# Kernel tuning notes

Hardware: AMD Instinct MI355X
Metric: run time of the kernel (lower is better)

## Reference

```python
import jax, jax.numpy as jnp
import numpy as np
from jax import lax

TOP_K = 4  # n_expert_per_token


def setup_inputs() -> dict:
    key = jax.random.key(0)
    ks = jax.random.split(key, 9)
    B, S, D, F, E = 2, 512, 1024, 2048, 32
    sD = 1.0 / np.sqrt(D)
    sF = 1.0 / np.sqrt(F)
    return {
        "x": jax.random.normal(ks[0], (B, S, D), jnp.float32),
        "gate_w": jax.random.normal(ks[1], (E, D), jnp.float32) * sD,
        "expert_bias": jax.random.normal(ks[2], (E,), jnp.float32) * 0.01,
        "wg": jax.random.normal(ks[3], (E, F, D), jnp.float32) * sD,
        "wu": jax.random.normal(ks[4], (E, F, D), jnp.float32) * sD,
        "wd": jax.random.normal(ks[5], (E, D, F), jnp.float32) * sF,
        "ws_g": jax.random.normal(ks[6], (F, D), jnp.float32) * sD,
        "ws_u": jax.random.normal(ks[7], (F, D), jnp.float32) * sD,
        "ws_d": jax.random.normal(ks[8], (D, F), jnp.float32) * sF,
    }


def _swiglu(xf, w_gate, w_up, w_down):
    # xf: [T, D]; w_gate/w_up: [F, D]; w_down: [D, F]
    h = jax.nn.silu(xf @ w_gate.T) * (xf @ w_up.T)
    return h @ w_down.T


def reference(x, gate_w, expert_bias, wg, wu, wd, ws_g, ws_u, ws_d):
    B, S, D = x.shape
    E = gate_w.shape[0]
    xf = x.reshape(-1, D)                      # [T, D]
    T = xf.shape[0]

    # shared expert (always active)
    shared = _swiglu(xf, ws_g, ws_u, ws_d)     # [T, D]

    # router: logits + load-balance bias, top-k, softmax over selected logits
    logits = xf @ gate_w.T + expert_bias       # [T, E]
    top_vals, top_idx = lax.top_k(logits, TOP_K)
    weights = jax.nn.softmax(top_vals, axis=-1)  # [T, K]

    # per-token combine weight for every expert (zero if not routed)
    cw = jnp.sum(jax.nn.one_hot(top_idx, E, dtype=weights.dtype) * weights[..., None], axis=1)  # [T, E]

    # dense-masked expert compute: scan over experts, accumulate weighted outputs
    def body(acc, p):
        wg_e, wu_e, wd_e, cw_e = p             # [F,D],[F,D],[D,F],[T]
        y = _swiglu(xf, wg_e, wu_e, wd_e)      # [T, D]
        return acc + cw_e[:, None] * y, None

    routed, _ = lax.scan(body, jnp.zeros_like(xf), (wg, wu, wd, cw.T))

    out = (shared + routed).reshape(B, S, D)

    # load stats (eval path; no bias update since training=False)
    counts = jnp.zeros((E,), jnp.float32).at[top_idx.reshape(-1)].add(1.0)
    load_balance = jnp.std(counts) / (jnp.mean(counts) + 1e-6)
    return out, counts, load_balance
```

## Files before the change

### kernel.cpp

```cpp
#include <hip/hip_runtime.h>
#include <hip/hip_bf16.h>
#include <math.h>

#define T_TOK 1024
#define DDIM  1024
#define FDIM  2048
#define NEXP  32
#define KTOP  4
#define ESH   33
#define RTOT  5120

#define WS_CNT   0
#define WS_NWORK 32
#define WS_OFF   34
#define WS_WL    68
#define WS_TOPI  324
#define WS_TOPW  4420
#define WS_LTOK  8516
#define WS_LW    13636
#define WS_H     18816

typedef __attribute__((ext_vector_type(8))) short short8;
typedef __attribute__((ext_vector_type(4))) float f32x4;

__device__ inline unsigned pack_bf16x2(float a, float b) {
  unsigned ua = __float_as_uint(a), ub = __float_as_uint(b);
  ua = (ua + 0x8000u) >> 16;
  ub = (ub + 0x8000u) & 0xFFFF0000u;
  return ua | ub;
}

__global__ void k_router(const float* __restrict__ x, const float* __restrict__ gw,
                         const float* __restrict__ bias, int* __restrict__ ws) {
  int t = blockIdx.x;
  int lane = threadIdx.x;
  int e = lane & 31, half = lane >> 5;
  const float* xh = x + (size_t)t * DDIM + half * (DDIM / 2);
  const float* gr = gw + (size_t)e * DDIM + half * (DDIM / 2);
  float acc = 0.f;
  for (int d = 0; d < DDIM / 2; d += 4) {
    float4 xv = *(const float4*)(xh + d);
    float4 gv = *(const float4*)(gr + d);
    acc += xv.x * gv.x + xv.y * gv.y + xv.z * gv.z + xv.w * gv.w;
  }
  acc += __shfl_xor(acc, 32, 64);
  __shared__ float lg[NEXP];
  if (lane < NEXP) lg[lane] = acc + bias[lane];
  __syncthreads();
  if (lane == 0) {
    int idx[KTOP]; float val[KTOP]; unsigned used = 0;
    for (int s = 0; s < KTOP; ++s) {
      float best = -1e30f; int bi = 0;
      for (int j = 0; j < NEXP; ++j)
        if (!((used >> j) & 1u) && lg[j] > best) { best = lg[j]; bi = j; }
      used |= 1u << bi; idx[s] = bi; val[s] = best;
    }
    float m = val[0], ssum = 0.f, w[KTOP];
    for (int s = 0; s < KTOP; ++s) { w[s] = __expf(val[s] - m); ssum += w[s]; }
    for (int s = 0; s < KTOP; ++s) {
      ws[WS_TOPI + t * KTOP + s] = idx[s];
      ((float*)ws)[WS_TOPW + t * KTOP + s] = w[s] / ssum;
      atomicAdd(&ws[WS_CNT + idx[s]], 1);
    }
  }
}

__global__ void k_post(int* __restrict__ ws, float* __restrict__ out) {
  __shared__ int off_s[ESH + 1];
  __shared__ int cur_s[ESH];
  int tid = threadIdx.x;
  if (tid == 0) {
    int o = 0;
    for (int e = 0; e < NEXP; ++e) { off_s[e] = o; o += ws[WS_CNT + e]; }
    off_s[32] = o; off_s[33] = o + T_TOK;
    int w = 0;
    for (int e = 0; e < ESH; ++e) {
      int n = (e < NEXP) ? ws[WS_CNT + e] : T_TOK;
      int tiles = (n + 31) >> 5;
      for (int mt = 0; mt < tiles; ++mt) ws[WS_WL + w++] = (e << 6) | mt;
    }
    ws[WS_NWORK] = w;
    for (int i = 0; i <= ESH; ++i) ws[WS_OFF + i] = off_s[i];
    float mean = 0.f;
    for (int e = 0; e < NEXP; ++e) mean += (float)ws[WS_CNT + e];
    mean *= (1.f / NEXP);
    float var = 0.f;
    for (int e = 0; e < NEXP; ++e) { float d = (float)ws[WS_CNT + e] - mean; var += d * d; }
    var *= (1.f / NEXP);
    for (int e = 0; e < NEXP; ++e) out[(size_t)T_TOK * DDIM + e] = (float)ws[WS_CNT + e];
    out[(size_t)T_TOK * DDIM + NEXP] = sqrtf(var) / (mean + 1e-6f);
  }
  if (tid < ESH) cur_s[tid] = 0;
  __syncthreads();
  if (tid < T_TOK) {
    for (int s = 0; s < KTOP; ++s) {
      int e = ws[WS_TOPI + tid * KTOP + s];
      int p = atomicAdd(&cur_s[e], 1);
      ws[WS_LTOK + off_s[e] + p] = tid;
      ((float*)ws)[WS_LW + off_s[e] + p] = ((const float*)ws)[WS_TOPW + tid * KTOP + s];
    }
    ws[WS_LTOK + off_s[32] + tid] = tid;
    ((float*)ws)[WS_LW + off_s[32] + tid] = 1.f;
  }
}

__global__ __launch_bounds__(256) void k_stage1(
    const float* __restrict__ x, const float* __restrict__ wg, const float* __restrict__ wu,
    const float* __restrict__ wsg, const float* __restrict__ wsu,
    const int* __restrict__ ws, __hip_bfloat16* __restrict__ H) {
  int wid = blockIdx.x;
  if (wid >= ws[WS_NWORK]) return;
  int wl = ws[WS_WL + wid];
  int e = wl >> 6, mt = wl & 63;
  int off_e = ws[WS_OFF + e];
  int n_e = ws[WS_OFF + e + 1] - off_e;
  int m0 = off_e + mt * 32;
  int nb = blockIdx.y * 64;
  const float* wgp = (e < NEXP) ? wg + (size_t)e * FDIM * DDIM : wsg;
  const float* wup = (e < NEXP) ? wu + (size_t)e * FDIM * DDIM : wsu;

  __shared__ int tok_s[32];
  __shared__ ushort a_s[8][32][8];
  __shared__ ushort bg_s[8][64][8];
  __shared__ ushort bu_s[8][64][8];

  int tid = threadIdx.x;
  if (tid < 32) {
    int idx = mt * 32 + tid;
    tok_s[tid] = ws[WS_LTOK + off_e + (idx < n_e ? idx : 0)];
  }
  __syncthreads();

  int kgA = tid & 7, mA = tid >> 3;
  const float* aptr = x + (size_t)tok_s[mA] * DDIM + kgA * 8;
  int kgB = tid & 7, nB = tid >> 3;
  f32x4 accg0 = {0,0,0,0}, accg1 = {0,0,0,0}, accu0 = {0,0,0,0}, accu1 = {0,0,0,0};
  int wave = tid >> 6, lane = tid & 63;
  int msub = wave & 1, npair = wave >> 1;
  int lm = lane & 15, lk = lane >> 4;

  for (int k0 = 0; k0 < DDIM; k0 += 64) {
    {
      float4 f0 = *(const float4*)(aptr + k0);
      float4 f1 = *(const float4*)(aptr + k0 + 4);
      uint4 p; p.x = pack_bf16x2(f0.x, f0.y); p.y = pack_bf16x2(f0.z, f0.w);
      p.z = pack_bf16x2(f1.x, f1.y); p.w = pack_bf16x2(f1.z, f1.w);
      *(uint4*)&a_s[kgA][mA][0] = p;
    }
#pragma unroll
    for (int r = 0; r < 2; ++r) {
      int n = nB + r * 32;
      const float* gsrc = wgp + (size_t)(nb + n) * DDIM + k0 + kgB * 8;
      float4 f0 = *(const float4*)gsrc; float4 f1 = *(const float4*)(gsrc + 4);
      uint4 p; p.x = pack_bf16x2(f0.x, f0.y); p.y = pack_bf16x2(f0.z, f0.w);
      p.z = pack_bf16x2(f1.x, f1.y); p.w = pack_bf16x2(f1.z, f1.w);
      *(uint4*)&bg_s[kgB][n][0] = p;
      const float* usrc = wup + (size_t)(nb + n) * DDIM + k0 + kgB * 8;
      f0 = *(const float4*)usrc; f1 = *(const float4*)(usrc + 4);
      p.x = pack_bf16x2(f0.x, f0.y); p.y = pack_bf16x2(f0.z, f0.w);
      p.z = pack_bf16x2(f1.x, f1.y); p.w = pack_bf16x2(f1.z, f1.w);
      *(uint4*)&bu_s[kgB][n][0] = p;
    }
    __syncthreads();
#pragma unroll
    for (int ks = 0; ks < 2; ++ks) {
      short8 av  = *(short8*)&a_s[ks * 4 + lk][msub * 16 + lm][0];
      short8 bg0 = *(short8*)&bg_s[ks * 4 + lk][npair * 32 + lm][0];
      short8 bu0 = *(short8*)&bu_s[ks * 4 + lk][npair * 32 + lm][0];
      short8 bg1 = *(short8*)&bg_s[ks * 4 + lk][npair * 32 + 16 + lm][0];
      short8 bu1 = *(short8*)&bu_s[ks * 4 + lk][npair * 32 + 16 + lm][0];
      accg0 = __builtin_amdgcn_mfma_f32_16x16x32_bf16(av, bg0, accg0, 0, 0, 0);
      accu0 = __builtin_amdgcn_mfma_f32_16x16x32_bf16(av, bu0, accu0, 0, 0, 0);
      accg1 = __builtin_amdgcn_mfma_f32_16x16x32_bf16(av, bg1, accg1, 0, 0, 0);
      accu1 = __builtin_amdgcn_mfma_f32_16x16x32_bf16(av, bu1, accu1, 0, 0, 0);
    }
    __syncthreads();
  }
#pragma unroll
  for (int ns = 0; ns < 2; ++ns) {
    f32x4 g = ns ? accg1 : accg0;
    f32x4 u = ns ? accu1 : accu0;
#pragma unroll
    for (int r = 0; r < 4; ++r) {
      int lrow = msub * 16 + lk * 4 + r;
      if (mt * 32 + lrow < n_e) {
        float gv = g[r];
        float hv = (gv / (1.f + __expf(-gv))) * u[r];
        H[(size_t)(m0 + lrow) * FDIM + nb + npair * 32 + ns * 16 + lm] = __float2bfloat16(hv);
      }
    }
  }
}

__global__ __launch_bounds__(256) void k_stage2(
    const float* __restrict__ wd, const float* __restrict__ wsd,
    const int* __restrict__ ws, const __hip_bfloat16* __restrict__ H,
    float* __restrict__ out) {
  int wid = blockIdx.x;
  if (wid >= ws[WS_NWORK]) return;
  int wl = ws[WS_WL + wid];
  int e = wl >> 6, mt = wl & 63;
  int off_e = ws[WS_OFF + e];
  int n_e = ws[WS_OFF + e + 1] - off_e;
  int m0 = off_e + mt * 32;
  int nb = blockIdx.y * 64;
  const float* wdp = (e < NEXP) ? wd + (size_t)e * DDIM * FDIM : wsd;

  __shared__ int tok_s[32];
  __shared__ float w_s[32];
  __shared__ ushort a_s[8][32][8];
  __shared__ ushort b_s[8][64][8];

  int tid = threadIdx.x;
  if (tid < 32) {
    int idx = mt * 32 + tid;
    int cl = idx < n_e ? idx : 0;
    tok_s[tid] = ws[WS_LTOK + off_e + cl];
    w_s[tid]   = ((const float*)ws)[WS_LW + off_e + cl];
  }
  __syncthreads();

  int kgA = tid & 7, mA = tid >> 3;
  const __hip_bfloat16* aptr = H + (size_t)(m0 + mA) * FDIM + kgA * 8;
  int kgB = tid & 7, nB = tid >> 3;
  f32x4 acc0 = {0,0,0,0}, acc1 = {0,0,0,0};
  int wave = tid >> 6, lane = tid & 63;
  int msub = wave & 1, npair = wave >> 1;
  int lm = lane & 15, lk = lane >> 4;

  for (int k0 = 0; k0 < FDIM; k0 += 64) {
    *(uint4*)&a_s[kgA][mA][0] = *(const uint4*)(aptr + k0);
#pragma unroll
    for (int r = 0; r < 2; ++r) {
      int n = nB + r * 32;
      const float* src = wdp + (size_t)(nb + n) * FDIM + k0 + kgB * 8;
      float4 f0 = *(const float4*)src; float4 f1 = *(const float4*)(src + 4);
      uint4 p; p.x = pack_bf16x2(f0.x, f0.y); p.y = pack_bf16x2(f0.z, f0.w);
      p.z = pack_bf16x2(f1.x, f1.y); p.w = pack_bf16x2(f1.z, f1.w);
      *(uint4*)&b_s[kgB][n][0] = p;
    }
    __syncthreads();
#pragma unroll
    for (int ks = 0; ks < 2; ++ks) {
      short8 av = *(short8*)&a_s[ks * 4 + lk][msub * 16 + lm][0];
      short8 b0 = *(short8*)&b_s[ks * 4 + lk][npair * 32 + lm][0];
      short8 b1 = *(short8*)&b_s[ks * 4 + lk][npair * 32 + 16 + lm][0];
      acc0 = __builtin_amdgcn_mfma_f32_16x16x32_bf16(av, b0, acc0, 0, 0, 0);
      acc1 = __builtin_amdgcn_mfma_f32_16x16x32_bf16(av, b1, acc1, 0, 0, 0);
    }
    __syncthreads();
  }
#pragma unroll
  for (int ns = 0; ns < 2; ++ns) {
    f32x4 a = ns ? acc1 : acc0;
#pragma unroll
    for (int r = 0; r < 4; ++r) {
      int lrow = msub * 16 + lk * 4 + r;
      if (mt * 32 + lrow < n_e) {
        int t = tok_s[lrow];
        atomicAdd(&out[(size_t)t * DDIM + nb + npair * 32 + ns * 16 + lm], w_s[lrow] * a[r]);
      }
    }
  }
}

extern "C" void kernel_launch(void* const* d_in, const int* in_sizes, int n_in,
                              void* d_out, int out_size, void* d_ws, size_t ws_size,
                              hipStream_t stream) {
  const float* x    = (const float*)d_in[0];
  const float* gw   = (const float*)d_in[1];
  const float* bias = (const float*)d_in[2];
  const float* wg   = (const float*)d_in[3];
  const float* wu   = (const float*)d_in[4];
  const float* wd   = (const float*)d_in[5];
  const float* wsg  = (const float*)d_in[6];
  const float* wsu  = (const float*)d_in[7];
  const float* wsd  = (const float*)d_in[8];
  float* out = (float*)d_out;
  int* ws = (int*)d_ws;
  __hip_bfloat16* H = (__hip_bfloat16*)((char*)d_ws + (size_t)WS_H * 4);

  hipMemsetAsync(d_out, 0, (size_t)out_size * sizeof(float), stream);
  hipMemsetAsync(d_ws, 0, 32 * sizeof(int), stream);
  k_router<<<T_TOK, 64, 0, stream>>>(x, gw, bias, ws);
  k_post<<<1, 1024, 0, stream>>>(ws, out);
  k_stage1<<<dim3(224, 32), 256, 0, stream>>>(x, wg, wu, wsg, wsu, ws, H);
  k_stage2<<<dim3(224, 16), 256, 0, stream>>>(wd, wsd, ws, H, out);
}
```

Before: 1.224 ms.

## Enlarge expert GEMM M-tile to 256 tokens with swizzled LDS and 512 threads

Both expert GEMM stages now process 256 routed tokens per block instead of 32. Each of the 8 waves computes a 64x32 sub-tile, so every fp32 weight tile is loaded from HBM and converted to bf16 once per 256 tokens rather than once per 32. The shared-memory layout becomes row-major with an XOR swizzle, which is meant to avoid bank conflicts on the MFMA operand reads, and the work list and grid are sized for the larger tiles. In exchange, experts with few tokens leave large parts of each tile idle, there are fewer blocks to fill the GPU, and registers and LDS per block go up.

```diff
diff --git a/kernel.cpp b/kernel.cpp
--- a/kernel.cpp
+++ b/kernel.cpp
@@ -76,7 +76,7 @@
     int w = 0;
     for (int e = 0; e < ESH; ++e) {
       int n = (e < NEXP) ? ws[WS_CNT + e] : T_TOK;
-      int tiles = (n + 31) >> 5;
+      int tiles = (n + 255) >> 8;
       for (int mt = 0; mt < tiles; ++mt) ws[WS_WL + w++] = (e << 6) | mt;
     }
     ws[WS_NWORK] = w;
@@ -104,7 +104,7 @@
   }
 }
 
-__global__ __launch_bounds__(256) void k_stage1(
+__global__ __launch_bounds__(512, 4) void k_stage1(
     const float* __restrict__ x, const float* __restrict__ wg, const float* __restrict__ wu,
     const float* __restrict__ wsg, const float* __restrict__ wsu,
     const int* __restrict__ ws, __hip_bfloat16* __restrict__ H) {
@@ -114,85 +114,112 @@
   int e = wl >> 6, mt = wl & 63;
   int off_e = ws[WS_OFF + e];
   int n_e = ws[WS_OFF + e + 1] - off_e;
-  int m0 = off_e + mt * 32;
+  int m0 = off_e + mt * 256;
+  int rloc = n_e - mt * 256;
   int nb = blockIdx.y * 64;
   const float* wgp = (e < NEXP) ? wg + (size_t)e * FDIM * DDIM : wsg;
   const float* wup = (e < NEXP) ? wu + (size_t)e * FDIM * DDIM : wsu;
 
-  __shared__ int tok_s[32];
-  __shared__ ushort a_s[8][32][8];
-  __shared__ ushort bg_s[8][64][8];
-  __shared__ ushort bu_s[8][64][8];
+  __shared__ int tok_s[256];
+  __shared__ ushort a_s[256][64];
+  __shared__ ushort bg_s[64][64];
+  __shared__ ushort bu_s[64][64];
 
   int tid = threadIdx.x;
-  if (tid < 32) {
-    int idx = mt * 32 + tid;
+  if (tid < 256) {
+    int idx = mt * 256 + tid;
     tok_s[tid] = ws[WS_LTOK + off_e + (idx < n_e ? idx : 0)];
   }
   __syncthreads();
 
-  int kgA = tid & 7, mA = tid >> 3;
-  const float* aptr = x + (size_t)tok_s[mA] * DDIM + kgA * 8;
-  int kgB = tid & 7, nB = tid >> 3;
-  f32x4 accg0 = {0,0,0,0}, accg1 = {0,0,0,0}, accu0 = {0,0,0,0}, accu1 = {0,0,0,0};
+  int kg = tid & 7;
+  int rB = tid >> 3;
   int wave = tid >> 6, lane = tid & 63;
-  int msub = wave & 1, npair = wave >> 1;
+  int wm = wave >> 1, wn = wave & 1;
   int lm = lane & 15, lk = lane >> 4;
 
+  f32x4 accg[4][2], accu[4][2];
+#pragma unroll
+  for (int a = 0; a < 4; ++a)
+#pragma unroll
+    for (int b = 0; b < 2; ++b) {
+      accg[a][b] = (f32x4){0.f, 0.f, 0.f, 0.f};
+      accu[a][b] = (f32x4){0.f, 0.f, 0.f, 0.f};
+    }
+
+  unsigned aoff[4];
+#pragma unroll
+  for (int i = 0; i < 4; ++i)
+    aoff[i] = (unsigned)tok_s[rB + i * 64] * (DDIM * 4) + kg * 32;
+  unsigned boff = (unsigned)(nb + rB) * (DDIM * 4) + kg * 32;
+
   for (int k0 = 0; k0 < DDIM; k0 += 64) {
-    {
-      float4 f0 = *(const float4*)(aptr + k0);
-      float4 f1 = *(const float4*)(aptr + k0 + 4);
+#pragma unroll
+    for (int i = 0; i < 4; ++i) {
+      int m = rB + i * 64;
+      float4 f0 = *(const float4*)((const char*)x + aoff[i] + k0 * 4);
+      float4 f1 = *(const float4*)((const char*)x + aoff[i] + k0 * 4 + 16);
       uint4 p; p.x = pack_bf16x2(f0.x, f0.y); p.y = pack_bf16x2(f0.z, f0.w);
       p.z = pack_bf16x2(f1.x, f1.y); p.w = pack_bf16x2(f1.z, f1.w);
-      *(uint4*)&a_s[kgA][mA][0] = p;
-    }
-#pragma unroll
-    for (int r = 0; r < 2; ++r) {
-      int n = nB + r * 32;
-      const float* gsrc = wgp + (size_t)(nb + n) * DDIM + k0 + kgB * 8;
-      float4 f0 = *(const float4*)gsrc; float4 f1 = *(const float4*)(gsrc + 4);
+      *(uint4*)&a_s[m][(kg ^ (m & 7)) << 3] = p;
+    }
+    {
+      float4 f0 = *(const float4*)((const char*)wgp + boff + k0 * 4);
+      float4 f1 = *(const float4*)((const char*)wgp + boff + k0 * 4 + 16);
       uint4 p; p.x = pack_bf16x2(f0.x, f0.y); p.y = pack_bf16x2(f0.z, f0.w);
       p.z = pack_bf16x2(f1.x, f1.y); p.w = pack_bf16x2(f1.z, f1.w);
-      *(uint4*)&bg_s[kgB][n][0] = p;
-      const float* usrc = wup + (size_t)(nb + n) * DDIM + k0 + kgB * 8;
-      f0 = *(const float4*)usrc; f1 = *(const float4*)(usrc + 4);
+      *(uint4*)&bg_s[rB][(kg ^ (rB & 7)) << 3] = p;
+      f0 = *(const float4*)((const char*)wup + boff + k0 * 4);
+      f1 = *(const float4*)((const char*)wup + boff + k0 * 4 + 16);
       p.x = pack_bf16x2(f0.x, f0.y); p.y = pack_bf16x2(f0.z, f0.w);
       p.z = pack_bf16x2(f1.x, f1.y); p.w = pack_bf16x2(f1.z, f1.w);
-      *(uint4*)&bu_s[kgB][n][0] = p;
+      *(uint4*)&bu_s[rB][(kg ^ (rB & 7)) << 3] = p;
     }
     __syncthreads();
 #pragma unroll
     for (int ks = 0; ks < 2; ++ks) {
-      short8 av  = *(short8*)&a_s[ks * 4 + lk][msub * 16 + lm][0];
-      short8 bg0 = *(short8*)&bg_s[ks * 4 + lk][npair * 32 + lm][0];
-      short8 bu0 = *(short8*)&bu_s[ks * 4 + lk][npair * 32 + lm][0];
-      short8 bg1 = *(short8*)&bg_s[ks * 4 + lk][npair * 32 + 16 + lm][0];
-      short8 bu1 = *(short8*)&bu_s[ks * 4 + lk][npair * 32 + 16 + lm][0];
-      accg0 = __builtin_amdgcn_mfma_f32_16x16x32_bf16(av, bg0, accg0, 0, 0, 0);
-      accu0 = __builtin_amdgcn_mfma_f32_16x16x32_bf16(av, bu0, accu0, 0, 0, 0);
-      accg1 = __builtin_amdgcn_mfma_f32_16x16x32_bf16(av, bg1, accg1, 0, 0, 0);
-      accu1 = __builtin_amdgcn_mfma_f32_16x16x32_bf16(av, bu1, accu1, 0, 0, 0);
+      int c = ks * 4 + lk;
+      short8 av[4];
+#pragma unroll
+      for (int mf = 0; mf < 4; ++mf) {
+        int row = wm * 64 + mf * 16 + lm;
+        av[mf] = *(short8*)&a_s[row][(c ^ (row & 7)) << 3];
+      }
+      int n0 = wn * 32 + lm;
+      int sw = (c ^ (n0 & 7)) << 3;
+      short8 bg0 = *(short8*)&bg_s[n0][sw];
+      short8 bg1 = *(short8*)&bg_s[n0 + 16][sw];
+#pragma unroll
+      for (int mf = 0; mf < 4; ++mf) {
+        accg[mf][0] = __builtin_amdgcn_mfma_f32_16x16x32_bf16(av[mf], bg0, accg[mf][0], 0, 0, 0);
+        accg[mf][1] = __builtin_amdgcn_mfma_f32_16x16x32_bf16(av[mf], bg1, accg[mf][1], 0, 0, 0);
+      }
+      short8 bu0 = *(short8*)&bu_s[n0][sw];
+      short8 bu1 = *(short8*)&bu_s[n0 + 16][sw];
+#pragma unroll
+      for (int mf = 0; mf < 4; ++mf) {
+        accu[mf][0] = __builtin_amdgcn_mfma_f32_16x16x32_bf16(av[mf], bu0, accu[mf][0], 0, 0, 0);
+        accu[mf][1] = __builtin_amdgcn_mfma_f32_16x16x32_bf16(av[mf], bu1, accu[mf][1], 0, 0, 0);
+      }
     }
     __syncthreads();
   }
 #pragma unroll
-  for (int ns = 0; ns < 2; ++ns) {
-    f32x4 g = ns ? accg1 : accg0;
-    f32x4 u = ns ? accu1 : accu0;
-#pragma unroll
-    for (int r = 0; r < 4; ++r) {
-      int lrow = msub * 16 + lk * 4 + r;
-      if (mt * 32 + lrow < n_e) {
-        float gv = g[r];
-        float hv = (gv / (1.f + __expf(-gv))) * u[r];
-        H[(size_t)(m0 + lrow) * FDIM + nb + npair * 32 + ns * 16 + lm] = __float2bfloat16(hv);
-      }
-    }
-  }
-}
-
-__global__ __launch_bounds__(256) void k_stage2(
+  for (int mf = 0; mf < 4; ++mf)
+#pragma unroll
+    for (int nf = 0; nf < 2; ++nf)
+#pragma unroll
+      for (int r = 0; r < 4; ++r) {
+        int lrow = wm * 64 + mf * 16 + lk * 4 + r;
+        if (lrow < rloc) {
+          float gv = accg[mf][nf][r];
+          float hv = (gv / (1.f + __expf(-gv))) * accu[mf][nf][r];
+          H[(size_t)(m0 + lrow) * FDIM + nb + wn * 32 + nf * 16 + lm] = __float2bfloat16(hv);
+        }
+      }
+}
+
+__global__ __launch_bounds__(512, 4) void k_stage2(
     const float* __restrict__ wd, const float* __restrict__ wsd,
     const int* __restrict__ ws, const __hip_bfloat16* __restrict__ H,
     float* __restrict__ out) {
@@ -202,66 +229,92 @@
   int e = wl >> 6, mt = wl & 63;
   int off_e = ws[WS_OFF + e];
   int n_e = ws[WS_OFF + e + 1] - off_e;
-  int m0 = off_e + mt * 32;
+  int m0 = off_e + mt * 256;
+  int rloc = n_e - mt * 256;
   int nb = blockIdx.y * 64;
   const float* wdp = (e < NEXP) ? wd + (size_t)e * DDIM * FDIM : wsd;
 
-  __shared__ int tok_s[32];
-  __shared__ float w_s[32];
-  __shared__ ushort a_s[8][32][8];
-  __shared__ ushort b_s[8][64][8];
+  __shared__ int tok_s[256];
+  __shared__ float w_s[256];
+  __shared__ ushort a_s[256][64];
+  __shared__ ushort b_s[64][64];
 
   int tid = threadIdx.x;
-  if (tid < 32) {
-    int idx = mt * 32 + tid;
+  if (tid < 256) {
+    int idx = mt * 256 + tid;
     int cl = idx < n_e ? idx : 0;
     tok_s[tid] = ws[WS_LTOK + off_e + cl];
     w_s[tid]   = ((const float*)ws)[WS_LW + off_e + cl];
   }
   __syncthreads();
 
-  int kgA = tid & 7, mA = tid >> 3;
-  const __hip_bfloat16* aptr = H + (size_t)(m0 + mA) * FDIM + kgA * 8;
-  int kgB = tid & 7, nB = tid >> 3;
-  f32x4 acc0 = {0,0,0,0}, acc1 = {0,0,0,0};
+  int kg = tid & 7;
+  int rB = tid >> 3;
   int wave = tid >> 6, lane = tid & 63;
-  int msub = wave & 1, npair = wave >> 1;
+  int wm = wave >> 1, wn = wave & 1;
   int lm = lane & 15, lk = lane >> 4;
 
+  f32x4 acc[4][2];
+#pragma unroll
+  for (int a = 0; a < 4; ++a)
+#pragma unroll
+    for (int b = 0; b < 2; ++b) acc[a][b] = (f32x4){0.f, 0.f, 0.f, 0.f};
+
+  unsigned aoff[4];
+#pragma unroll
+  for (int i = 0; i < 4; ++i)
+    aoff[i] = (unsigned)(m0 + rB + i * 64) * (FDIM * 2) + kg * 16;
+  unsigned boff = (unsigned)(nb + rB) * (FDIM * 4) + kg * 32;
+
   for (int k0 = 0; k0 < FDIM; k0 += 64) {
-    *(uint4*)&a_s[kgA][mA][0] = *(const uint4*)(aptr + k0);
-#pragma unroll
-    for (int r = 0; r < 2; ++r) {
-      int n = nB + r * 32;
-      const float* src = wdp + (size_t)(nb + n) * FDIM + k0 + kgB * 8;
-      float4 f0 = *(const float4*)src; float4 f1 = *(const float4*)(src + 4);
+#pragma unroll
+    for (int i = 0; i < 4; ++i) {
+      int m = rB + i * 64;
+      uint4 p = *(const uint4*)((const char*)H + aoff[i] + k0 * 2);
+      *(uint4*)&a_s[m][(kg ^ (m & 7)) << 3] = p;
+    }
+    {
+      float4 f0 = *(const float4*)((const char*)wdp + boff + k0 * 4);
+      float4 f1 = *(const float4*)((const char*)wdp + boff + k0 * 4 + 16);
       uint4 p; p.x = pack_bf16x2(f0.x, f0.y); p.y = pack_bf16x2(f0.z, f0.w);
       p.z = pack_bf16x2(f1.x, f1.y); p.w = pack_bf16x2(f1.z, f1.w);
-      *(uint4*)&b_s[kgB][n][0] = p;
+      *(uint4*)&b_s[rB][(kg ^ (rB & 7)) << 3] = p;
     }
     __syncthreads();
 #pragma unroll
     for (int ks = 0; ks < 2; ++ks) {
-      short8 av = *(short8*)&a_s[ks * 4 + lk][msub * 16 + lm][0];
-      short8 b0 = *(short8*)&b_s[ks * 4 + lk][npair * 32 + lm][0];
-      short8 b1 = *(short8*)&b_s[ks * 4 + lk][npair * 32 + 16 + lm][0];
-      acc0 = __builtin_amdgcn_mfma_f32_16x16x32_bf16(av, b0, acc0, 0, 0, 0);
-      acc1 = __builtin_amdgcn_mfma_f32_16x16x32_bf16(av, b1, acc1, 0, 0, 0);
+      int c = ks * 4 + lk;
+      short8 av[4];
+#pragma unroll
+      for (int mf = 0; mf < 4; ++mf) {
+        int row = wm * 64 + mf * 16 + lm;
+        av[mf] = *(short8*)&a_s[row][(c ^ (row & 7)) << 3];
+      }
+      int n0 = wn * 32 + lm;
+      int sw = (c ^ (n0 & 7)) << 3;
+      short8 b0 = *(short8*)&b_s[n0][sw];
+      short8 b1 = *(short8*)&b_s[n0 + 16][sw];
+#pragma unroll
+      for (int mf = 0; mf < 4; ++mf) {
+        acc[mf][0] = __builtin_amdgcn_mfma_f32_16x16x32_bf16(av[mf], b0, acc[mf][0], 0, 0, 0);
+        acc[mf][1] = __builtin_amdgcn_mfma_f32_16x16x32_bf16(av[mf], b1, acc[mf][1], 0, 0, 0);
+      }
     }
     __syncthreads();
   }
 #pragma unroll
-  for (int ns = 0; ns < 2; ++ns) {
-    f32x4 a = ns ? acc1 : acc0;
-#pragma unroll
-    for (int r = 0; r < 4; ++r) {
-      int lrow = msub * 16 + lk * 4 + r;
-      if (mt * 32 + lrow < n_e) {
-        int t = tok_s[lrow];
-        atomicAdd(&out[(size_t)t * DDIM + nb + npair * 32 + ns * 16 + lm], w_s[lrow] * a[r]);
-      }
-    }
-  }
+  for (int mf = 0; mf < 4; ++mf)
+#pragma unroll
+    for (int nf = 0; nf < 2; ++nf)
+#pragma unroll
+      for (int r = 0; r < 4; ++r) {
+        int lrow = wm * 64 + mf * 16 + lk * 4 + r;
+        if (lrow < rloc) {
+          int t = tok_s[lrow];
+          atomicAdd(&out[(size_t)t * DDIM + nb + wn * 32 + nf * 16 + lm],
+                    w_s[lrow] * acc[mf][nf][r]);
+        }
+      }
 }
 
 extern "C" void kernel_launch(void* const* d_in, const int* in_sizes, int n_in,
@@ -284,6 +337,6 @@
   hipMemsetAsync(d_ws, 0, 32 * sizeof(int), stream);
   k_router<<<T_TOK, 64, 0, stream>>>(x, gw, bias, ws);
   k_post<<<1, 1024, 0, stream>>>(ws, out);
-  k_stage1<<<dim3(224, 32), 256, 0, stream>>>(x, wg, wu, wsg, wsu, ws, H);
-  k_stage2<<<dim3(224, 16), 256, 0, stream>>>(wd, wsd, ws, H, out);
-}
+  k_stage1<<<dim3(64, 32), 512, 0, stream>>>(x, wg, wu, wsg, wsu, ws, H);
+  k_stage2<<<dim3(64, 16), 512, 0, stream>>>(wd, wsd, ws, H, out);
+}
```

Result: faster. 1.042 ms (-14.9%).
